# Kernel optimization log

Hardware: AMD Instinct MI355X
Metric: run time of the kernel (lower is better)

## Reference

```python
import jax, jax.numpy as jnp
import numpy as np

B, P, F = 8, 8192, 32          # clouds, points per cloud, feature dim
RATIO, R, K = 0.25, 0.2, 64    # fps ratio, ball radius, max neighbors
M = int(P * RATIO)             # centroids per cloud


def setup_inputs() -> dict:
    key = jax.random.key(0)
    ks = jax.random.split(key, 6)
    pos = jax.random.uniform(ks[0], (B * P, 3), dtype=jnp.float32)
    batch = jnp.repeat(jnp.arange(B, dtype=jnp.int32), P)
    x = jax.random.normal(ks[1], (B * P, F), dtype=jnp.float32)

    def lin(k, i, o):
        return jax.random.normal(k, (i, o), dtype=jnp.float32) * (1.0 / np.sqrt(i))

    return {
        "pos": pos, "batch": batch, "x": x,
        "W1": lin(ks[2], F + 3, 64), "b1": jnp.zeros((64,), jnp.float32),
        "W2": lin(ks[3], 64, 64),    "b2": jnp.zeros((64,), jnp.float32),
        "W3": lin(ks[4], 64, 128),   "b3": jnp.zeros((128,), jnp.float32),
    }


def _fps(pos_b):
    """Farthest point sampling on one cloud [P,3] -> [M] indices (start at 0)."""
    d0 = jnp.full((P,), jnp.inf, pos_b.dtype)

    def step(carry, _):
        dists, last = carry
        d = jnp.sum((pos_b - pos_b[last]) ** 2, axis=-1)
        dists = jnp.minimum(dists, d)
        nxt = jnp.argmax(dists).astype(jnp.int32)
        return (dists, nxt), nxt

    _, idx = jax.lax.scan(step, (d0, jnp.int32(0)), None, length=M - 1)
    return jnp.concatenate([jnp.zeros((1,), jnp.int32), idx])


def reference(pos, batch, x, W1, b1, W2, b2, W3, b3):
    posb = pos.reshape(B, P, 3)
    xb = x.reshape(B, P, F)

    # --- FPS: pick M pivot points per cloud ---
    idx = jax.vmap(_fps)(posb)                                   # [B,M]
    cent = jnp.take_along_axis(posb, idx[..., None], axis=1)     # [B,M,3]

    # --- radius ball query: up to K neighbors within R (lowest indices first) ---
    d2 = jnp.sum((cent[:, :, None, :] - posb[:, None, :, :]) ** 2, axis=-1)  # [B,M,P]
    in_ball = d2 <= R * R
    nb = jnp.sort(jnp.where(in_ball, jnp.arange(P)[None, None, :], P), axis=-1)[..., :K]
    valid = nb < P                                               # [B,M,K]
    nb_safe = jnp.where(valid, nb, 0)

    # --- gather -> point_filter MLP -> masked max aggregation (PointNetConv) ---
    pos_j = jax.vmap(lambda p, i: p[i])(posb, nb_safe)           # [B,M,K,3]
    x_j = jax.vmap(lambda f, i: f[i])(xb, nb_safe)               # [B,M,K,F]
    msg = jnp.concatenate([x_j, pos_j - cent[:, :, None, :]], axis=-1)  # [B,M,K,F+3]
    h = jax.nn.relu(msg @ W1 + b1)
    h = jax.nn.relu(h @ W2 + b2)
    h = jax.nn.relu(h @ W3 + b3)                                 # [B,M,K,128]
    neg = jnp.finfo(h.dtype).min
    h = jnp.where(valid[..., None], h, neg)
    out = jnp.max(h, axis=2)  # every centroid is its own neighbor -> non-empty

    centr_batch = jnp.repeat(jnp.arange(B, dtype=batch.dtype), M)
    return cent.reshape(B * M, 3), out.reshape(B * M, 128), centr_batch
```

## Files before the change

### kernel.cpp

```cpp
#include <hip/hip_runtime.h>
#include <stdint.h>
#include <math.h>

constexpr int kB = 8;
constexpr int kP = 8192;
constexpr int kF = 32;
constexpr int kM = 2048;
constexpr int kK = 64;
constexpr int kO = 128;

typedef float v2f __attribute__((ext_vector_type(2)));
typedef _Float16 h8 __attribute__((ext_vector_type(8)));
typedef float f4v __attribute__((ext_vector_type(4)));

__device__ __forceinline__ float dist2(float ax, float ay, float az,
                                       float bx, float by, float bz) {
#pragma clang fp contract(off)
    float dx = ax - bx, dy = ay - by, dz = az - bz;
    return (dx * dx + dy * dy) + dz * dz;
}

template <int CTRL>
__device__ __forceinline__ void dpp_max_step(unsigned int& khi, unsigned int& klo) {
    unsigned int ohi = (unsigned int)__builtin_amdgcn_update_dpp(
        0, (int)khi, CTRL, 0xf, 0xf, true);
    unsigned int olo = (unsigned int)__builtin_amdgcn_update_dpp(
        0, (int)klo, CTRL, 0xf, 0xf, true);
    bool take = (ohi > khi) || (ohi == khi && olo > klo);
    khi = take ? ohi : khi;
    klo = take ? olo : klo;
}

__global__ void init_kernel(int* __restrict__ prog) {
    if (threadIdx.x < 128) prog[threadIdx.x] = 0;
}

union SharedU {
    struct {
        float sxp[kP], syp[kP], szp[kP];
        unsigned short widx[kM];
        unsigned long long part[2][4];
    } f;
    struct {
        _Float16 A0[256][72];
        _Float16 A1[256][72];
        _Float16 Wt1[64][72];
        _Float16 Wt2[64][72];
        _Float16 Wt3[128][72];
        float bias[256];
        float red[4][4][128];
        int   s_nb[4][kK];
        int   s_cnt[4];
    } c;
};

__global__ __launch_bounds__(256, 1) void mega_kernel(
    const float* __restrict__ pos, const float* __restrict__ x,
    const float* __restrict__ W1, const float* __restrict__ b1,
    const float* __restrict__ W2, const float* __restrict__ b2,
    const float* __restrict__ W3, const float* __restrict__ b3,
    unsigned int* __restrict__ stage, int* __restrict__ prog,
    float* __restrict__ cent_out, float* __restrict__ feat_out,
    float* __restrict__ batch_out) {
    __shared__ SharedU sh;

    const int tid = threadIdx.x;
    const int wave = tid >> 6, lane = tid & 63;

    if (blockIdx.x < (unsigned)kB) {
        const int b = blockIdx.x;
        const float* pb = pos + (size_t)b * kP * 3;

        v2f px2[16], py2[16], pz2[16], dd2[16];
#pragma unroll
        for (int q = 0; q < 32; ++q) {
            int i = tid + q * 256;
            float X = pb[i * 3 + 0];
            float Y = pb[i * 3 + 1];
            float Z = pb[i * 3 + 2];
            sh.f.sxp[i] = X; sh.f.syp[i] = Y; sh.f.szp[i] = Z;
            if (q & 1) { px2[q >> 1].y = X; py2[q >> 1].y = Y; pz2[q >> 1].y = Z; }
            else       { px2[q >> 1].x = X; py2[q >> 1].x = Y; pz2[q >> 1].x = Z; }
        }
#pragma unroll
        for (int q = 0; q < 16; ++q) dd2[q] = (v2f){INFINITY, INFINITY};

        if (tid == 0) sh.f.widx[0] = 0;
        __syncthreads();

        float lx = sh.f.sxp[0], ly = sh.f.syp[0], lz = sh.f.szp[0];
        if (tid == 0) {
            size_t o = (size_t)(b * kM) * 3;
            __hip_atomic_store(&stage[o + 0], __float_as_uint(lx),
                               __ATOMIC_RELAXED, __HIP_MEMORY_SCOPE_AGENT);
            __hip_atomic_store(&stage[o + 1], __float_as_uint(ly),
                               __ATOMIC_RELAXED, __HIP_MEMORY_SCOPE_AGENT);
            __hip_atomic_store(&stage[o + 2], __float_as_uint(lz),
                               __ATOMIC_RELAXED, __HIP_MEMORY_SCOPE_AGENT);
            __hip_atomic_store(&prog[b * 16], 1,
                               __ATOMIC_RELEASE, __HIP_MEMORY_SCOPE_AGENT);
        }

        for (int m = 1; m < kM; ++m) {
            v2f lxv = {lx, lx}, lyv = {ly, ly}, lzv = {lz, lz};
#pragma unroll
            for (int q = 0; q < 16; ++q) {
#pragma clang fp contract(off)
                v2f dx = px2[q] - lxv;
                v2f dy = py2[q] - lyv;
                v2f dz = pz2[q] - lzv;
                v2f d2 = (dx * dx + dy * dy) + dz * dz;
                dd2[q].x = fminf(dd2[q].x, d2.x);
                dd2[q].y = fminf(dd2[q].y, d2.y);
            }

            v2f t0 = {fmaxf(dd2[0].x, dd2[0].y), fmaxf(dd2[1].x, dd2[1].y)};
            v2f t1 = {fmaxf(dd2[2].x, dd2[2].y), fmaxf(dd2[3].x, dd2[3].y)};
            v2f t2 = {fmaxf(dd2[4].x, dd2[4].y), fmaxf(dd2[5].x, dd2[5].y)};
            v2f t3 = {fmaxf(dd2[6].x, dd2[6].y), fmaxf(dd2[7].x, dd2[7].y)};
            v2f t4 = {fmaxf(dd2[8].x, dd2[8].y), fmaxf(dd2[9].x, dd2[9].y)};
            v2f t5 = {fmaxf(dd2[10].x, dd2[10].y), fmaxf(dd2[11].x, dd2[11].y)};
            v2f t6 = {fmaxf(dd2[12].x, dd2[12].y), fmaxf(dd2[13].x, dd2[13].y)};
            v2f t7 = {fmaxf(dd2[14].x, dd2[14].y), fmaxf(dd2[15].x, dd2[15].y)};
            float u0 = fmaxf(fmaxf(t0.x, t0.y), fmaxf(t1.x, t1.y));
            float u1 = fmaxf(fmaxf(t2.x, t2.y), fmaxf(t3.x, t3.y));
            float u2 = fmaxf(fmaxf(t4.x, t4.y), fmaxf(t5.x, t5.y));
            float u3 = fmaxf(fmaxf(t6.x, t6.y), fmaxf(t7.x, t7.y));
            float bv = fmaxf(fmaxf(u0, u1), fmaxf(u2, u3));

            int lqs[4];
#pragma unroll
            for (int g = 0; g < 4; ++g) {
                int t = 64;
#pragma unroll
                for (int s = 7; s >= 0; --s) {
                    int sl = g * 8 + s;
                    float v = (sl & 1) ? dd2[sl >> 1].y : dd2[sl >> 1].x;
                    t = (v == bv) ? sl : t;
                }
                lqs[g] = t;
            }
            int bq = lqs[3];
            bq = (lqs[2] < 64) ? lqs[2] : bq;
            bq = (lqs[1] < 64) ? lqs[1] : bq;
            bq = (lqs[0] < 64) ? lqs[0] : bq;

            unsigned int bidx = (unsigned int)(tid + bq * 256);
            unsigned int khi = __float_as_uint(bv);
            unsigned int klo = (unsigned int)(~bidx);

            dpp_max_step<0x111>(khi, klo);
            dpp_max_step<0x112>(khi, klo);
            dpp_max_step<0x114>(khi, klo);
            dpp_max_step<0x118>(khi, klo);
            dpp_max_step<0x142>(khi, klo);
            dpp_max_step<0x143>(khi, klo);
            if (lane == 63)
                sh.f.part[m & 1][wave] = ((unsigned long long)khi << 32) | klo;
            __syncthreads();

            unsigned long long k = sh.f.part[m & 1][0];
#pragma unroll
            for (int w = 1; w < 4; ++w) {
                unsigned long long o = sh.f.part[m & 1][w];
                if (o > k) k = o;
            }
            unsigned int wi = ~(unsigned int)k;
            lx = sh.f.sxp[wi]; ly = sh.f.syp[wi]; lz = sh.f.szp[wi];
            if (tid == 0) sh.f.widx[m] = (unsigned short)wi;

            if ((m & 31) == 31) {
                int m0 = m - 31;
                if (tid < 96) {
                    int mm = m0 + tid / 3;
                    int comp = tid % 3;
                    unsigned int w2 = (mm == m) ? wi
                                                : (unsigned int)sh.f.widx[mm];
                    float v = (comp == 0) ? sh.f.sxp[w2]
                            : (comp == 1) ? sh.f.syp[w2] : sh.f.szp[w2];
                    __hip_atomic_store(&stage[(size_t)(b * kM + mm) * 3 + comp],
                                       __float_as_uint(v),
                                       __ATOMIC_RELAXED, __HIP_MEMORY_SCOPE_AGENT);
                }
                __syncthreads();
                if (tid == 0)
                    __hip_atomic_store(&prog[b * 16], m + 1,
                                       __ATOMIC_RELEASE, __HIP_MEMORY_SCOPE_AGENT);
            }
        }
        __syncthreads();

#pragma unroll
        for (int q = 0; q < kM / 256; ++q) {
            int i = tid + q * 256;
            unsigned int wi = sh.f.widx[i];
            size_t o = (size_t)(b * kM + i) * 3;
            cent_out[o + 0] = sh.f.sxp[wi];
            cent_out[o + 1] = sh.f.syp[wi];
            cent_out[o + 2] = sh.f.szp[wi];
        }
        return;
    }

    const int i = (int)blockIdx.x - kB;
    const int b = i & 7;
    const int cl0 = (i >> 3) * 4;

    for (int idx = tid; idx < 64 * 64; idx += 256) {
        int n = idx & 63, kk = idx >> 6;
        sh.c.Wt1[n][kk] = (_Float16)((kk < 35) ? W1[kk * 64 + n] : 0.0f);
        sh.c.Wt2[n][kk] = (_Float16)W2[kk * 64 + n];
    }
    for (int idx = tid; idx < 64 * 128; idx += 256) {
        int n = idx & 127, kk = idx >> 7;
        sh.c.Wt3[n][kk] = (_Float16)W3[kk * 128 + n];
    }
    sh.c.bias[tid] = (tid < 64) ? b1[tid] : (tid < 128) ? b2[tid - 64]
                                                        : b3[tid - 128];

    if (tid == 0) {
        int p;
        while ((p = __hip_atomic_load(&prog[b * 16], __ATOMIC_ACQUIRE,
                                      __HIP_MEMORY_SCOPE_AGENT)) < cl0 + 4) {
            if (cl0 + 4 - p > 128) __builtin_amdgcn_s_sleep(64);
            else                   __builtin_amdgcn_s_sleep(8);
        }
    }
    __syncthreads();

    const int c = b * kM + cl0 + wave;
    float cx = __uint_as_float(__hip_atomic_load(&stage[(size_t)c * 3 + 0],
                   __ATOMIC_RELAXED, __HIP_MEMORY_SCOPE_AGENT));
    float cy = __uint_as_float(__hip_atomic_load(&stage[(size_t)c * 3 + 1],
                   __ATOMIC_RELAXED, __HIP_MEMORY_SCOPE_AGENT));
    float cz = __uint_as_float(__hip_atomic_load(&stage[(size_t)c * 3 + 2],
                   __ATOMIC_RELAXED, __HIP_MEMORY_SCOPE_AGENT));
    {
        const float R2 = (float)(0.2 * 0.2);
        const float* pb = pos + (size_t)b * kP * 3;
        int cnt = 0;
        for (int p0 = 0; p0 < kP && cnt < kK; p0 += 64) {
            int idx = p0 + lane;
            float X = pb[idx * 3 + 0], Y = pb[idx * 3 + 1], Z = pb[idx * 3 + 2];
            float d2 = dist2(X, Y, Z, cx, cy, cz);
            bool in = d2 <= R2;
            unsigned long long mask = __ballot(in);
            int rank = __popcll(mask & ((1ull << lane) - 1ull));
            if (in && cnt + rank < kK) sh.c.s_nb[wave][cnt + rank] = idx;
            cnt = min(cnt + (int)__popcll(mask), kK);
        }
        if (lane == 0) { sh.c.s_cnt[wave] = cnt; batch_out[c] = (float)b; }
    }
    __syncthreads();
    const int cntw = sh.c.s_cnt[wave];

    {
        int k = lane;
        if (k < cntw) {
            int n = sh.c.s_nb[wave][k];
            const float4* xr4 = (const float4*)(x + ((size_t)b * kP + n) * kF);
#pragma unroll
            for (int t = 0; t < 4; ++t) {
                float4 a4 = xr4[2 * t], c4 = xr4[2 * t + 1];
                h8 o = {(_Float16)a4.x, (_Float16)a4.y, (_Float16)a4.z,
                        (_Float16)a4.w, (_Float16)c4.x, (_Float16)c4.y,
                        (_Float16)c4.z, (_Float16)c4.w};
                *(h8*)&sh.c.A0[tid][t * 8] = o;
            }
            float dx = pos[((size_t)b * kP + n) * 3 + 0] - cx;
            float dy = pos[((size_t)b * kP + n) * 3 + 1] - cy;
            float dz = pos[((size_t)b * kP + n) * 3 + 2] - cz;
            h8 o4 = {(_Float16)dx, (_Float16)dy, (_Float16)dz,
                     (_Float16)0.f, (_Float16)0.f, (_Float16)0.f,
                     (_Float16)0.f, (_Float16)0.f};
            *(h8*)&sh.c.A0[tid][32] = o4;
            h8 z = {};
            *(h8*)&sh.c.A0[tid][40] = z;
            *(h8*)&sh.c.A0[tid][48] = z;
            *(h8*)&sh.c.A0[tid][56] = z;
        } else {
            h8 z = {};
#pragma unroll
            for (int t = 0; t < 8; ++t) *(h8*)&sh.c.A0[tid][t * 8] = z;
        }
    }
    __syncthreads();

    const int m16 = lane & 15, quad = lane >> 4;

    {
        h8 bf[4][2];
#pragma unroll
        for (int nt = 0; nt < 4; ++nt)
#pragma unroll
            for (int kc = 0; kc < 2; ++kc)
                bf[nt][kc] = *(const h8*)&sh.c.Wt1[nt * 16 + m16][kc * 32 + quad * 8];
#pragma unroll
        for (int mt = 0; mt < 4; ++mt) {
            int m0 = wave * 64 + mt * 16;
            h8 a0 = *(const h8*)&sh.c.A0[m0 + m16][quad * 8];
            h8 a1 = *(const h8*)&sh.c.A0[m0 + m16][32 + quad * 8];
#pragma unroll
            for (int nt = 0; nt < 4; ++nt) {
                f4v acc = {0.f, 0.f, 0.f, 0.f};
                acc = __builtin_amdgcn_mfma_f32_16x16x32_f16(a0, bf[nt][0], acc, 0, 0, 0);
                acc = __builtin_amdgcn_mfma_f32_16x16x32_f16(a1, bf[nt][1], acc, 0, 0, 0);
                int n = nt * 16 + m16;
                float bb = sh.c.bias[n];
#pragma unroll
                for (int r = 0; r < 4; ++r)
                    sh.c.A1[m0 + quad * 4 + r][n] =
                        (_Float16)fmaxf(acc[r] + bb, 0.0f);
            }
        }
    }
    __syncthreads();

    {
        h8 bf[4][2];
#pragma unroll
        for (int nt = 0; nt < 4; ++nt)
#pragma unroll
            for (int kc = 0; kc < 2; ++kc)
                bf[nt][kc] = *(const h8*)&sh.c.Wt2[nt * 16 + m16][kc * 32 + quad * 8];
#pragma unroll
        for (int mt = 0; mt < 4; ++mt) {
            int m0 = wave * 64 + mt * 16;
            h8 a0 = *(const h8*)&sh.c.A1[m0 + m16][quad * 8];
            h8 a1 = *(const h8*)&sh.c.A1[m0 + m16][32 + quad * 8];
#pragma unroll
            for (int nt = 0; nt < 4; ++nt) {
                f4v acc = {0.f, 0.f, 0.f, 0.f};
                acc = __builtin_amdgcn_mfma_f32_16x16x32_f16(a0, bf[nt][0], acc, 0, 0, 0);
                acc = __builtin_amdgcn_mfma_f32_16x16x32_f16(a1, bf[nt][1], acc, 0, 0, 0);
                int n = nt * 16 + m16;
                float bb = sh.c.bias[64 + n];
#pragma unroll
                for (int r = 0; r < 4; ++r)
                    sh.c.A0[m0 + quad * 4 + r][n] =
                        (_Float16)fmaxf(acc[r] + bb, 0.0f);
            }
        }
    }
    __syncthreads();

    {
        h8 bf[8][2];
#pragma unroll
        for (int nt = 0; nt < 8; ++nt)
#pragma unroll
            for (int kc = 0; kc < 2; ++kc)
                bf[nt][kc] = *(const h8*)&sh.c.Wt3[nt * 16 + m16][kc * 32 + quad * 8];
        float best[8];
#pragma unroll
        for (int nt = 0; nt < 8; ++nt) best[nt] = -INFINITY;
#pragma unroll
        for (int mt = 0; mt < 4; ++mt) {
            int m0 = wave * 64 + mt * 16;
            h8 a0 = *(const h8*)&sh.c.A0[m0 + m16][quad * 8];
            h8 a1 = *(const h8*)&sh.c.A0[m0 + m16][32 + quad * 8];
#pragma unroll
            for (int nt = 0; nt < 8; ++nt) {
                f4v acc = {0.f, 0.f, 0.f, 0.f};
                acc = __builtin_amdgcn_mfma_f32_16x16x32_f16(a0, bf[nt][0], acc, 0, 0, 0);
                acc = __builtin_amdgcn_mfma_f32_16x16x32_f16(a1, bf[nt][1], acc, 0, 0, 0);
                int n = nt * 16 + m16;
                float bb = sh.c.bias[128 + n];
#pragma unroll
                for (int r = 0; r < 4; ++r) {
                    int krow = mt * 16 + quad * 4 + r;
                    float v = fmaxf(acc[r] + bb, 0.0f);
                    if (krow < cntw) best[nt] = fmaxf(best[nt], v);
                }
            }
        }
#pragma unroll
        for (int nt = 0; nt < 8; ++nt)
            sh.c.red[wave][quad][nt * 16 + m16] = best[nt];
    }
    __syncthreads();

    {
        int w2 = tid >> 6, n = tid & 63;
#pragma unroll
        for (int h = 0; h < 2; ++h) {
            int n2 = n + h * 64;
            float o = fmaxf(fmaxf(sh.c.red[w2][0][n2], sh.c.red[w2][1][n2]),
                            fmaxf(sh.c.red[w2][2][n2], sh.c.red[w2][3][n2]));
            feat_out[(size_t)(b * kM + cl0 + w2) * kO + n2] = o;
        }
    }
}

extern "C" void kernel_launch(void* const* d_in, const int* in_sizes, int n_in,
                              void* d_out, int out_size, void* d_ws, size_t ws_size,
                              hipStream_t stream) {
    const float* pos = (const float*)d_in[0];
    const float* x  = (const float*)d_in[2];
    const float* W1 = (const float*)d_in[3];
    const float* b1 = (const float*)d_in[4];
    const float* W2 = (const float*)d_in[5];
    const float* b2 = (const float*)d_in[6];
    const float* W3 = (const float*)d_in[7];
    const float* b3 = (const float*)d_in[8];

    float* out = (float*)d_out;
    float* cent_out  = out;
    float* feat_out  = out + (size_t)kB * kM * 3;
    float* batch_out = out + (size_t)kB * kM * (3 + kO);

    char* ws = (char*)d_ws;
    int* prog           = (int*)ws;
    unsigned int* stage = (unsigned int*)(ws + 512);

    init_kernel<<<1, 128, 0, stream>>>(prog);
    mega_kernel<<<kB + (kB * kM) / 4, 256, 0, stream>>>(
        pos, x, W1, b1, W2, b2, W3, b3, stage, prog,
        cent_out, feat_out, batch_out);
}
```

Measured before the change: 2.153 ms.

## Use 512-thread blocks so FPS spreads points across eight waves

Block size goes from 256 to 512 threads. The FPS blocks now hold 16 points per thread instead of 32, and the cross-wave reduction covers eight partial results. Consumer blocks run their existing four-wave work with the extra four waves idle apart from helping load weights. The aim is to cut per-iteration latency in the serial FPS loop, which likely dominates. The cost is a larger cross-wave reduction per step and idle waves in the consumer blocks, which may lower their occupancy.

```diff
diff --git a/kernel.cpp b/kernel.cpp
--- a/kernel.cpp
+++ b/kernel.cpp
@@ -39,7 +39,7 @@
     struct {
         float sxp[kP], syp[kP], szp[kP];
         unsigned short widx[kM];
-        unsigned long long part[2][4];
+        unsigned long long part[2][8];
     } f;
     struct {
         _Float16 A0[256][72];
@@ -54,7 +54,7 @@
     } c;
 };
 
-__global__ __launch_bounds__(256, 1) void mega_kernel(
+__global__ __launch_bounds__(512, 2) void mega_kernel(
     const float* __restrict__ pos, const float* __restrict__ x,
     const float* __restrict__ W1, const float* __restrict__ b1,
     const float* __restrict__ W2, const float* __restrict__ b2,
@@ -71,10 +71,10 @@
         const int b = blockIdx.x;
         const float* pb = pos + (size_t)b * kP * 3;
 
-        v2f px2[16], py2[16], pz2[16], dd2[16];
-#pragma unroll
-        for (int q = 0; q < 32; ++q) {
-            int i = tid + q * 256;
+        v2f px2[8], py2[8], pz2[8], dd2[8];
+#pragma unroll
+        for (int q = 0; q < 16; ++q) {
+            int i = tid + q * 512;
             float X = pb[i * 3 + 0];
             float Y = pb[i * 3 + 1];
             float Z = pb[i * 3 + 2];
@@ -83,7 +83,7 @@
             else       { px2[q >> 1].x = X; py2[q >> 1].x = Y; pz2[q >> 1].x = Z; }
         }
 #pragma unroll
-        for (int q = 0; q < 16; ++q) dd2[q] = (v2f){INFINITY, INFINITY};
+        for (int q = 0; q < 8; ++q) dd2[q] = (v2f){INFINITY, INFINITY};
 
         if (tid == 0) sh.f.widx[0] = 0;
         __syncthreads();
@@ -104,7 +104,7 @@
         for (int m = 1; m < kM; ++m) {
             v2f lxv = {lx, lx}, lyv = {ly, ly}, lzv = {lz, lz};
 #pragma unroll
-            for (int q = 0; q < 16; ++q) {
+            for (int q = 0; q < 8; ++q) {
 #pragma clang fp contract(off)
                 v2f dx = px2[q] - lxv;
                 v2f dy = py2[q] - lyv;
@@ -118,19 +118,13 @@
             v2f t1 = {fmaxf(dd2[2].x, dd2[2].y), fmaxf(dd2[3].x, dd2[3].y)};
             v2f t2 = {fmaxf(dd2[4].x, dd2[4].y), fmaxf(dd2[5].x, dd2[5].y)};
             v2f t3 = {fmaxf(dd2[6].x, dd2[6].y), fmaxf(dd2[7].x, dd2[7].y)};
-            v2f t4 = {fmaxf(dd2[8].x, dd2[8].y), fmaxf(dd2[9].x, dd2[9].y)};
-            v2f t5 = {fmaxf(dd2[10].x, dd2[10].y), fmaxf(dd2[11].x, dd2[11].y)};
-            v2f t6 = {fmaxf(dd2[12].x, dd2[12].y), fmaxf(dd2[13].x, dd2[13].y)};
-            v2f t7 = {fmaxf(dd2[14].x, dd2[14].y), fmaxf(dd2[15].x, dd2[15].y)};
             float u0 = fmaxf(fmaxf(t0.x, t0.y), fmaxf(t1.x, t1.y));
             float u1 = fmaxf(fmaxf(t2.x, t2.y), fmaxf(t3.x, t3.y));
-            float u2 = fmaxf(fmaxf(t4.x, t4.y), fmaxf(t5.x, t5.y));
-            float u3 = fmaxf(fmaxf(t6.x, t6.y), fmaxf(t7.x, t7.y));
-            float bv = fmaxf(fmaxf(u0, u1), fmaxf(u2, u3));
-
-            int lqs[4];
-#pragma unroll
-            for (int g = 0; g < 4; ++g) {
+            float bv = fmaxf(u0, u1);
+
+            int lqs[2];
+#pragma unroll
+            for (int g = 0; g < 2; ++g) {
                 int t = 64;
 #pragma unroll
                 for (int s = 7; s >= 0; --s) {
@@ -140,12 +134,9 @@
                 }
                 lqs[g] = t;
             }
-            int bq = lqs[3];
-            bq = (lqs[2] < 64) ? lqs[2] : bq;
-            bq = (lqs[1] < 64) ? lqs[1] : bq;
-            bq = (lqs[0] < 64) ? lqs[0] : bq;
-
-            unsigned int bidx = (unsigned int)(tid + bq * 256);
+            int bq = (lqs[0] < 64) ? lqs[0] : lqs[1];
+
+            unsigned int bidx = (unsigned int)(tid + bq * 512);
             unsigned int khi = __float_as_uint(bv);
             unsigned int klo = (unsigned int)(~bidx);
 
@@ -159,12 +150,22 @@
                 sh.f.part[m & 1][wave] = ((unsigned long long)khi << 32) | klo;
             __syncthreads();
 
-            unsigned long long k = sh.f.part[m & 1][0];
-#pragma unroll
-            for (int w = 1; w < 4; ++w) {
-                unsigned long long o = sh.f.part[m & 1][w];
-                if (o > k) k = o;
-            }
+            unsigned long long p0 = sh.f.part[m & 1][0];
+            unsigned long long p1 = sh.f.part[m & 1][1];
+            unsigned long long p2 = sh.f.part[m & 1][2];
+            unsigned long long p3 = sh.f.part[m & 1][3];
+            unsigned long long p4 = sh.f.part[m & 1][4];
+            unsigned long long p5 = sh.f.part[m & 1][5];
+            unsigned long long p6 = sh.f.part[m & 1][6];
+            unsigned long long p7 = sh.f.part[m & 1][7];
+            unsigned long long a0 = p0 > p1 ? p0 : p1;
+            unsigned long long a1 = p2 > p3 ? p2 : p3;
+            unsigned long long a2 = p4 > p5 ? p4 : p5;
+            unsigned long long a3 = p6 > p7 ? p6 : p7;
+            unsigned long long b0 = a0 > a1 ? a0 : a1;
+            unsigned long long b1h = a2 > a3 ? a2 : a3;
+            unsigned long long k = b0 > b1h ? b0 : b1h;
+
             unsigned int wi = ~(unsigned int)k;
             lx = sh.f.sxp[wi]; ly = sh.f.syp[wi]; lz = sh.f.szp[wi];
             if (tid == 0) sh.f.widx[m] = (unsigned short)wi;
@@ -191,8 +192,8 @@
         __syncthreads();
 
 #pragma unroll
-        for (int q = 0; q < kM / 256; ++q) {
-            int i = tid + q * 256;
+        for (int q = 0; q < kM / 512; ++q) {
+            int i = tid + q * 512;
             unsigned int wi = sh.f.widx[i];
             size_t o = (size_t)(b * kM + i) * 3;
             cent_out[o + 0] = sh.f.sxp[wi];
@@ -206,17 +207,18 @@
     const int b = i & 7;
     const int cl0 = (i >> 3) * 4;
 
-    for (int idx = tid; idx < 64 * 64; idx += 256) {
+    for (int idx = tid; idx < 64 * 64; idx += 512) {
         int n = idx & 63, kk = idx >> 6;
         sh.c.Wt1[n][kk] = (_Float16)((kk < 35) ? W1[kk * 64 + n] : 0.0f);
         sh.c.Wt2[n][kk] = (_Float16)W2[kk * 64 + n];
     }
-    for (int idx = tid; idx < 64 * 128; idx += 256) {
+    for (int idx = tid; idx < 64 * 128; idx += 512) {
         int n = idx & 127, kk = idx >> 7;
         sh.c.Wt3[n][kk] = (_Float16)W3[kk * 128 + n];
     }
-    sh.c.bias[tid] = (tid < 64) ? b1[tid] : (tid < 128) ? b2[tid - 64]
-                                                        : b3[tid - 128];
+    if (tid < 256)
+        sh.c.bias[tid] = (tid < 64) ? b1[tid] : (tid < 128) ? b2[tid - 64]
+                                                            : b3[tid - 128];
 
     if (tid == 0) {
         int p;
@@ -228,14 +230,15 @@
     }
     __syncthreads();
 
-    const int c = b * kM + cl0 + wave;
-    float cx = __uint_as_float(__hip_atomic_load(&stage[(size_t)c * 3 + 0],
-                   __ATOMIC_RELAXED, __HIP_MEMORY_SCOPE_AGENT));
-    float cy = __uint_as_float(__hip_atomic_load(&stage[(size_t)c * 3 + 1],
-                   __ATOMIC_RELAXED, __HIP_MEMORY_SCOPE_AGENT));
-    float cz = __uint_as_float(__hip_atomic_load(&stage[(size_t)c * 3 + 2],
-                   __ATOMIC_RELAXED, __HIP_MEMORY_SCOPE_AGENT));
-    {
+    float cx = 0.f, cy = 0.f, cz = 0.f;
+    if (wave < 4) {
+        const int c = b * kM + cl0 + wave;
+        cx = __uint_as_float(__hip_atomic_load(&stage[(size_t)c * 3 + 0],
+                 __ATOMIC_RELAXED, __HIP_MEMORY_SCOPE_AGENT));
+        cy = __uint_as_float(__hip_atomic_load(&stage[(size_t)c * 3 + 1],
+                 __ATOMIC_RELAXED, __HIP_MEMORY_SCOPE_AGENT));
+        cz = __uint_as_float(__hip_atomic_load(&stage[(size_t)c * 3 + 2],
+                 __ATOMIC_RELAXED, __HIP_MEMORY_SCOPE_AGENT));
         const float R2 = (float)(0.2 * 0.2);
         const float* pb = pos + (size_t)b * kP * 3;
         int cnt = 0;
@@ -252,9 +255,9 @@
         if (lane == 0) { sh.c.s_cnt[wave] = cnt; batch_out[c] = (float)b; }
     }
     __syncthreads();
-    const int cntw = sh.c.s_cnt[wave];
-
-    {
+    const int cntw = (wave < 4) ? sh.c.s_cnt[wave] : 0;
+
+    if (wave < 4) {
         int k = lane;
         if (k < cntw) {
             int n = sh.c.s_nb[wave][k];
@@ -288,7 +291,7 @@
 
     const int m16 = lane & 15, quad = lane >> 4;
 
-    {
+    if (wave < 4) {
         h8 bf[4][2];
 #pragma unroll
         for (int nt = 0; nt < 4; ++nt)
@@ -316,7 +319,7 @@
     }
     __syncthreads();
 
-    {
+    if (wave < 4) {
         h8 bf[4][2];
 #pragma unroll
         for (int nt = 0; nt < 4; ++nt)
@@ -344,7 +347,7 @@
     }
     __syncthreads();
 
-    {
+    if (wave < 4) {
         h8 bf[8][2];
 #pragma unroll
         for (int nt = 0; nt < 8; ++nt)
@@ -380,7 +383,7 @@
     }
     __syncthreads();
 
-    {
+    if (tid < 256) {
         int w2 = tid >> 6, n = tid & 63;
 #pragma unroll
         for (int h = 0; h < 2; ++h) {
@@ -414,7 +417,7 @@
     unsigned int* stage = (unsigned int*)(ws + 512);
 
     init_kernel<<<1, 128, 0, stream>>>(prog);
-    mega_kernel<<<kB + (kB * kM) / 4, 256, 0, stream>>>(
+    mega_kernel<<<kB + (kB * kM) / 4, 512, 0, stream>>>(
         pos, x, W1, b1, W2, b2, W3, b3, stage, prog,
         cent_out, feat_out, batch_out);
 }
```

Result: slower. 2.222 ms (+3.2%).

## Run two FPS clouds per block to share barriers and interleave reductions

Applied to the files above, without the earlier changes.

Each FPS block now processes two clouds at once, holding both clouds' points and distances in registers and doing both update/argmax reductions before a single shared barrier per iteration. The second cloud's winning point is read from global memory instead of LDS. The aim is to amortize the per-iteration barrier and hide latency by interleaving two independent serial chains, freeing four blocks for the consumer stage. The cost is doubled register pressure, more VALU work per iteration on one CU, and global loads on the critical path for cloud B.

```diff
diff --git a/kernel.cpp b/kernel.cpp
--- a/kernel.cpp
+++ b/kernel.cpp
@@ -31,6 +31,59 @@
     klo = take ? olo : klo;
 }
 
+#define FPS_UPDATE_REDUCE(PX, PY, PZ, DD, LX, LY, LZ, KHI, KLO, WIOUT_UNUSED) \
+    {                                                                          \
+        v2f lxv = {LX, LX}, lyv = {LY, LY}, lzv = {LZ, LZ};                    \
+        _Pragma("unroll")                                                      \
+        for (int q = 0; q < 16; ++q) {                                         \
+            _Pragma("clang fp contract(off)")                                  \
+            v2f dx = PX[q] - lxv;                                              \
+            v2f dy = PY[q] - lyv;                                              \
+            v2f dz = PZ[q] - lzv;                                              \
+            v2f d2 = (dx * dx + dy * dy) + dz * dz;                            \
+            DD[q].x = fminf(DD[q].x, d2.x);                                    \
+            DD[q].y = fminf(DD[q].y, d2.y);                                    \
+        }                                                                      \
+        v2f t0 = {fmaxf(DD[0].x, DD[0].y), fmaxf(DD[1].x, DD[1].y)};           \
+        v2f t1 = {fmaxf(DD[2].x, DD[2].y), fmaxf(DD[3].x, DD[3].y)};           \
+        v2f t2 = {fmaxf(DD[4].x, DD[4].y), fmaxf(DD[5].x, DD[5].y)};           \
+        v2f t3 = {fmaxf(DD[6].x, DD[6].y), fmaxf(DD[7].x, DD[7].y)};           \
+        v2f t4 = {fmaxf(DD[8].x, DD[8].y), fmaxf(DD[9].x, DD[9].y)};           \
+        v2f t5 = {fmaxf(DD[10].x, DD[10].y), fmaxf(DD[11].x, DD[11].y)};       \
+        v2f t6 = {fmaxf(DD[12].x, DD[12].y), fmaxf(DD[13].x, DD[13].y)};       \
+        v2f t7 = {fmaxf(DD[14].x, DD[14].y), fmaxf(DD[15].x, DD[15].y)};       \
+        float u0 = fmaxf(fmaxf(t0.x, t0.y), fmaxf(t1.x, t1.y));                \
+        float u1 = fmaxf(fmaxf(t2.x, t2.y), fmaxf(t3.x, t3.y));                \
+        float u2 = fmaxf(fmaxf(t4.x, t4.y), fmaxf(t5.x, t5.y));                \
+        float u3 = fmaxf(fmaxf(t6.x, t6.y), fmaxf(t7.x, t7.y));                \
+        float bv = fmaxf(fmaxf(u0, u1), fmaxf(u2, u3));                        \
+        int lqs[4];                                                            \
+        _Pragma("unroll")                                                      \
+        for (int g = 0; g < 4; ++g) {                                          \
+            int t = 64;                                                        \
+            _Pragma("unroll")                                                  \
+            for (int s = 7; s >= 0; --s) {                                     \
+                int sl = g * 8 + s;                                            \
+                float v = (sl & 1) ? DD[sl >> 1].y : DD[sl >> 1].x;            \
+                t = (v == bv) ? sl : t;                                        \
+            }                                                                  \
+            lqs[g] = t;                                                        \
+        }                                                                      \
+        int bq = lqs[3];                                                       \
+        bq = (lqs[2] < 64) ? lqs[2] : bq;                                      \
+        bq = (lqs[1] < 64) ? lqs[1] : bq;                                      \
+        bq = (lqs[0] < 64) ? lqs[0] : bq;                                      \
+        unsigned int bidx = (unsigned int)(tid + bq * 256);                    \
+        KHI = __float_as_uint(bv);                                             \
+        KLO = (unsigned int)(~bidx);                                           \
+        dpp_max_step<0x111>(KHI, KLO);                                         \
+        dpp_max_step<0x112>(KHI, KLO);                                         \
+        dpp_max_step<0x114>(KHI, KLO);                                         \
+        dpp_max_step<0x118>(KHI, KLO);                                         \
+        dpp_max_step<0x142>(KHI, KLO);                                         \
+        dpp_max_step<0x143>(KHI, KLO);                                         \
+    }
+
 __global__ void init_kernel(int* __restrict__ prog) {
     if (threadIdx.x < 128) prog[threadIdx.x] = 0;
 }
@@ -38,8 +91,9 @@
 union SharedU {
     struct {
         float sxp[kP], syp[kP], szp[kP];
-        unsigned short widx[kM];
-        unsigned long long part[2][4];
+        unsigned short widxA[kM], widxB[kM];
+        unsigned long long partA[2][4];
+        unsigned long long partB[2][4];
     } f;
     struct {
         _Float16 A0[256][72];
@@ -67,125 +121,124 @@
     const int tid = threadIdx.x;
     const int wave = tid >> 6, lane = tid & 63;
 
-    if (blockIdx.x < (unsigned)kB) {
-        const int b = blockIdx.x;
-        const float* pb = pos + (size_t)b * kP * 3;
-
-        v2f px2[16], py2[16], pz2[16], dd2[16];
+    if (blockIdx.x < 4u) {
+        const int bA = (int)blockIdx.x * 2, bB = bA + 1;
+        const float* pA = pos + (size_t)bA * kP * 3;
+        const float* pB = pos + (size_t)bB * kP * 3;
+
+        v2f pxA[16], pyA[16], pzA[16], ddA[16];
+        v2f pxB[16], pyB[16], pzB[16], ddB[16];
 #pragma unroll
         for (int q = 0; q < 32; ++q) {
             int i = tid + q * 256;
-            float X = pb[i * 3 + 0];
-            float Y = pb[i * 3 + 1];
-            float Z = pb[i * 3 + 2];
-            sh.f.sxp[i] = X; sh.f.syp[i] = Y; sh.f.szp[i] = Z;
-            if (q & 1) { px2[q >> 1].y = X; py2[q >> 1].y = Y; pz2[q >> 1].y = Z; }
-            else       { px2[q >> 1].x = X; py2[q >> 1].x = Y; pz2[q >> 1].x = Z; }
-        }
-#pragma unroll
-        for (int q = 0; q < 16; ++q) dd2[q] = (v2f){INFINITY, INFINITY};
-
-        if (tid == 0) sh.f.widx[0] = 0;
+            float XA = pA[i * 3 + 0], YA = pA[i * 3 + 1], ZA = pA[i * 3 + 2];
+            sh.f.sxp[i] = XA; sh.f.syp[i] = YA; sh.f.szp[i] = ZA;
+            float XB = pB[i * 3 + 0], YB = pB[i * 3 + 1], ZB = pB[i * 3 + 2];
+            if (q & 1) {
+                pxA[q >> 1].y = XA; pyA[q >> 1].y = YA; pzA[q >> 1].y = ZA;
+                pxB[q >> 1].y = XB; pyB[q >> 1].y = YB; pzB[q >> 1].y = ZB;
+            } else {
+                pxA[q >> 1].x = XA; pyA[q >> 1].x = YA; pzA[q >> 1].x = ZA;
+                pxB[q >> 1].x = XB; pyB[q >> 1].x = YB; pzB[q >> 1].x = ZB;
+            }
+        }
+#pragma unroll
+        for (int q = 0; q < 16; ++q) {
+            ddA[q] = (v2f){INFINITY, INFINITY};
+            ddB[q] = (v2f){INFINITY, INFINITY};
+        }
+
+        if (tid == 0) { sh.f.widxA[0] = 0; sh.f.widxB[0] = 0; }
         __syncthreads();
 
-        float lx = sh.f.sxp[0], ly = sh.f.syp[0], lz = sh.f.szp[0];
+        float lxA = sh.f.sxp[0], lyA = sh.f.syp[0], lzA = sh.f.szp[0];
+        float lxB = pB[0], lyB = pB[1], lzB = pB[2];
         if (tid == 0) {
-            size_t o = (size_t)(b * kM) * 3;
-            __hip_atomic_store(&stage[o + 0], __float_as_uint(lx),
-                               __ATOMIC_RELAXED, __HIP_MEMORY_SCOPE_AGENT);
-            __hip_atomic_store(&stage[o + 1], __float_as_uint(ly),
-                               __ATOMIC_RELAXED, __HIP_MEMORY_SCOPE_AGENT);
-            __hip_atomic_store(&stage[o + 2], __float_as_uint(lz),
-                               __ATOMIC_RELAXED, __HIP_MEMORY_SCOPE_AGENT);
-            __hip_atomic_store(&prog[b * 16], 1,
+            size_t oA = (size_t)(bA * kM) * 3, oB = (size_t)(bB * kM) * 3;
+            __hip_atomic_store(&stage[oA + 0], __float_as_uint(lxA),
+                               __ATOMIC_RELAXED, __HIP_MEMORY_SCOPE_AGENT);
+            __hip_atomic_store(&stage[oA + 1], __float_as_uint(lyA),
+                               __ATOMIC_RELAXED, __HIP_MEMORY_SCOPE_AGENT);
+            __hip_atomic_store(&stage[oA + 2], __float_as_uint(lzA),
+                               __ATOMIC_RELAXED, __HIP_MEMORY_SCOPE_AGENT);
+            __hip_atomic_store(&stage[oB + 0], __float_as_uint(lxB),
+                               __ATOMIC_RELAXED, __HIP_MEMORY_SCOPE_AGENT);
+            __hip_atomic_store(&stage[oB + 1], __float_as_uint(lyB),
+                               __ATOMIC_RELAXED, __HIP_MEMORY_SCOPE_AGENT);
+            __hip_atomic_store(&stage[oB + 2], __float_as_uint(lzB),
+                               __ATOMIC_RELAXED, __HIP_MEMORY_SCOPE_AGENT);
+            __hip_atomic_store(&prog[bA * 16], 1,
                                __ATOMIC_RELEASE, __HIP_MEMORY_SCOPE_AGENT);
+            __hip_atomic_store(&prog[bB * 16], 1,
+                               __ATOMIC_RELEASE, __HIP_MEMORY_SCOPE_AGENT);
         }
 
         for (int m = 1; m < kM; ++m) {
-            v2f lxv = {lx, lx}, lyv = {ly, ly}, lzv = {lz, lz};
-#pragma unroll
-            for (int q = 0; q < 16; ++q) {
-#pragma clang fp contract(off)
-                v2f dx = px2[q] - lxv;
-                v2f dy = py2[q] - lyv;
-                v2f dz = pz2[q] - lzv;
-                v2f d2 = (dx * dx + dy * dy) + dz * dz;
-                dd2[q].x = fminf(dd2[q].x, d2.x);
-                dd2[q].y = fminf(dd2[q].y, d2.y);
-            }
-
-            v2f t0 = {fmaxf(dd2[0].x, dd2[0].y), fmaxf(dd2[1].x, dd2[1].y)};
-            v2f t1 = {fmaxf(dd2[2].x, dd2[2].y), fmaxf(dd2[3].x, dd2[3].y)};
-            v2f t2 = {fmaxf(dd2[4].x, dd2[4].y), fmaxf(dd2[5].x, dd2[5].y)};
-            v2f t3 = {fmaxf(dd2[6].x, dd2[6].y), fmaxf(dd2[7].x, dd2[7].y)};
-            v2f t4 = {fmaxf(dd2[8].x, dd2[8].y), fmaxf(dd2[9].x, dd2[9].y)};
-            v2f t5 = {fmaxf(dd2[10].x, dd2[10].y), fmaxf(dd2[11].x, dd2[11].y)};
-            v2f t6 = {fmaxf(dd2[12].x, dd2[12].y), fmaxf(dd2[13].x, dd2[13].y)};
-            v2f t7 = {fmaxf(dd2[14].x, dd2[14].y), fmaxf(dd2[15].x, dd2[15].y)};
-            float u0 = fmaxf(fmaxf(t0.x, t0.y), fmaxf(t1.x, t1.y));
-            float u1 = fmaxf(fmaxf(t2.x, t2.y), fmaxf(t3.x, t3.y));
-            float u2 = fmaxf(fmaxf(t4.x, t4.y), fmaxf(t5.x, t5.y));
-            float u3 = fmaxf(fmaxf(t6.x, t6.y), fmaxf(t7.x, t7.y));
-            float bv = fmaxf(fmaxf(u0, u1), fmaxf(u2, u3));
-
-            int lqs[4];
-#pragma unroll
-            for (int g = 0; g < 4; ++g) {
-                int t = 64;
-#pragma unroll
-                for (int s = 7; s >= 0; --s) {
-                    int sl = g * 8 + s;
-                    float v = (sl & 1) ? dd2[sl >> 1].y : dd2[sl >> 1].x;
-                    t = (v == bv) ? sl : t;
-                }
-                lqs[g] = t;
-            }
-            int bq = lqs[3];
-            bq = (lqs[2] < 64) ? lqs[2] : bq;
-            bq = (lqs[1] < 64) ? lqs[1] : bq;
-            bq = (lqs[0] < 64) ? lqs[0] : bq;
-
-            unsigned int bidx = (unsigned int)(tid + bq * 256);
-            unsigned int khi = __float_as_uint(bv);
-            unsigned int klo = (unsigned int)(~bidx);
-
-            dpp_max_step<0x111>(khi, klo);
-            dpp_max_step<0x112>(khi, klo);
-            dpp_max_step<0x114>(khi, klo);
-            dpp_max_step<0x118>(khi, klo);
-            dpp_max_step<0x142>(khi, klo);
-            dpp_max_step<0x143>(khi, klo);
-            if (lane == 63)
-                sh.f.part[m & 1][wave] = ((unsigned long long)khi << 32) | klo;
+            unsigned int khiA, kloA, khiB, kloB;
+            FPS_UPDATE_REDUCE(pxA, pyA, pzA, ddA, lxA, lyA, lzA, khiA, kloA, 0)
+            FPS_UPDATE_REDUCE(pxB, pyB, pzB, ddB, lxB, lyB, lzB, khiB, kloB, 0)
+            if (lane == 63) {
+                sh.f.partA[m & 1][wave] =
+                    ((unsigned long long)khiA << 32) | kloA;
+                sh.f.partB[m & 1][wave] =
+                    ((unsigned long long)khiB << 32) | kloB;
+            }
             __syncthreads();
 
-            unsigned long long k = sh.f.part[m & 1][0];
+            unsigned long long kb = sh.f.partB[m & 1][0];
 #pragma unroll
             for (int w = 1; w < 4; ++w) {
-                unsigned long long o = sh.f.part[m & 1][w];
-                if (o > k) k = o;
-            }
-            unsigned int wi = ~(unsigned int)k;
-            lx = sh.f.sxp[wi]; ly = sh.f.syp[wi]; lz = sh.f.szp[wi];
-            if (tid == 0) sh.f.widx[m] = (unsigned short)wi;
+                unsigned long long o = sh.f.partB[m & 1][w];
+                if (o > kb) kb = o;
+            }
+            unsigned int wiB = ~(unsigned int)kb;
+            lxB = pB[wiB * 3 + 0]; lyB = pB[wiB * 3 + 1]; lzB = pB[wiB * 3 + 2];
+
+            unsigned long long ka = sh.f.partA[m & 1][0];
+#pragma unroll
+            for (int w = 1; w < 4; ++w) {
+                unsigned long long o = sh.f.partA[m & 1][w];
+                if (o > ka) ka = o;
+            }
+            unsigned int wiA = ~(unsigned int)ka;
+            lxA = sh.f.sxp[wiA]; lyA = sh.f.syp[wiA]; lzA = sh.f.szp[wiA];
+
+            if (tid == 0) {
+                sh.f.widxA[m] = (unsigned short)wiA;
+                sh.f.widxB[m] = (unsigned short)wiB;
+            }
 
             if ((m & 31) == 31) {
                 int m0 = m - 31;
-                if (tid < 96) {
-                    int mm = m0 + tid / 3;
-                    int comp = tid % 3;
-                    unsigned int w2 = (mm == m) ? wi
-                                                : (unsigned int)sh.f.widx[mm];
-                    float v = (comp == 0) ? sh.f.sxp[w2]
-                            : (comp == 1) ? sh.f.syp[w2] : sh.f.szp[w2];
-                    __hip_atomic_store(&stage[(size_t)(b * kM + mm) * 3 + comp],
-                                       __float_as_uint(v),
-                                       __ATOMIC_RELAXED, __HIP_MEMORY_SCOPE_AGENT);
+                if (tid < 192) {
+                    int s = tid / 3, comp = tid % 3;
+                    int mm = m0 + (s & 31);
+                    float v;
+                    int cloud;
+                    if (s < 32) {
+                        unsigned int w2 = (mm == m) ? wiA
+                                        : (unsigned int)sh.f.widxA[mm];
+                        v = (comp == 0) ? sh.f.sxp[w2]
+                          : (comp == 1) ? sh.f.syp[w2] : sh.f.szp[w2];
+                        cloud = bA;
+                    } else {
+                        unsigned int w2 = (mm == m) ? wiB
+                                        : (unsigned int)sh.f.widxB[mm];
+                        v = pB[w2 * 3 + comp];
+                        cloud = bB;
+                    }
+                    __hip_atomic_store(
+                        &stage[(size_t)(cloud * kM + mm) * 3 + comp],
+                        __float_as_uint(v),
+                        __ATOMIC_RELAXED, __HIP_MEMORY_SCOPE_AGENT);
                 }
                 __syncthreads();
-                if (tid == 0)
-                    __hip_atomic_store(&prog[b * 16], m + 1,
+                if (tid == 0) {
+                    __hip_atomic_store(&prog[bA * 16], m + 1,
                                        __ATOMIC_RELEASE, __HIP_MEMORY_SCOPE_AGENT);
+                    __hip_atomic_store(&prog[bB * 16], m + 1,
+                                       __ATOMIC_RELEASE, __HIP_MEMORY_SCOPE_AGENT);
+                }
             }
         }
         __syncthreads();
@@ -193,16 +246,21 @@
 #pragma unroll
         for (int q = 0; q < kM / 256; ++q) {
             int i = tid + q * 256;
-            unsigned int wi = sh.f.widx[i];
-            size_t o = (size_t)(b * kM + i) * 3;
-            cent_out[o + 0] = sh.f.sxp[wi];
-            cent_out[o + 1] = sh.f.syp[wi];
-            cent_out[o + 2] = sh.f.szp[wi];
+            unsigned int wA = sh.f.widxA[i];
+            size_t oA = (size_t)(bA * kM + i) * 3;
+            cent_out[oA + 0] = sh.f.sxp[wA];
+            cent_out[oA + 1] = sh.f.syp[wA];
+            cent_out[oA + 2] = sh.f.szp[wA];
+            unsigned int wB = sh.f.widxB[i];
+            size_t oB = (size_t)(bB * kM + i) * 3;
+            cent_out[oB + 0] = pB[wB * 3 + 0];
+            cent_out[oB + 1] = pB[wB * 3 + 1];
+            cent_out[oB + 2] = pB[wB * 3 + 2];
         }
         return;
     }
 
-    const int i = (int)blockIdx.x - kB;
+    const int i = (int)blockIdx.x - 4;
     const int b = i & 7;
     const int cl0 = (i >> 3) * 4;
 
@@ -414,7 +472,7 @@
     unsigned int* stage = (unsigned int*)(ws + 512);
 
     init_kernel<<<1, 128, 0, stream>>>(prog);
-    mega_kernel<<<kB + (kB * kM) / 4, 256, 0, stream>>>(
+    mega_kernel<<<4 + (kB * kM) / 4, 256, 0, stream>>>(
         pos, x, W1, b1, W2, b2, W3, b3, stage, prog,
         cent_out, feat_out, batch_out);
 }
```

Result: slower. 4.825 ms (+124.1%).
